# Optimization experiments

Hardware: AMD Instinct MI355X
Metric: run time of the kernel (lower is better)

The kernel has to match this reference:

```python
import jax, jax.numpy as jnp
import numpy as np
from jax import lax


def _conv(x, w, b):
    # x: [B, Cin, H, W], w: [Cout, Cin, 3, 3] -> [B, Cout, H, W] (SAME padding)
    y = lax.conv_general_dilated(x, w, (1, 1), 'SAME',
                                 dimension_numbers=('NCHW', 'OIHW', 'NCHW'))
    return y + b[None, :, None, None]


def _cell_step(h, c, x, w, b):
    gates = _conv(jnp.concatenate([x, h], axis=1), w, b)  # [B, 4, H, W]
    i, f, o, g = jnp.split(gates, 4, axis=1)
    c = jax.nn.sigmoid(f) * c + jax.nn.sigmoid(i) * jnp.tanh(g)
    h = jax.nn.sigmoid(o) * jnp.tanh(c)
    return h, c


def setup_inputs() -> dict:
    key = jax.random.key(0)
    k1, k2, k3 = jax.random.split(key, 3)
    T, B, C, H, W = 20, 1, 1, 1024, 1024
    data = jax.random.normal(k1, (T, B, C, H, W), dtype=jnp.float32)
    enc_w = jax.random.normal(k2, (4, 2, 3, 3), dtype=jnp.float32) * 0.3
    enc_b = jnp.zeros((4,), dtype=jnp.float32)
    dec_w = jax.random.normal(k3, (4, 2, 3, 3), dtype=jnp.float32) * 0.3
    dec_b = jnp.zeros((4,), dtype=jnp.float32)
    return {"data": data, "enc_w": enc_w, "enc_b": enc_b,
            "dec_w": dec_w, "dec_b": dec_b,
            "epoch": 0, "T_en": 20, "T_de": 20}


def reference(data, enc_w, enc_b, dec_w, dec_b, epoch, T_en, T_de):
    B, C, H, W = data.shape[1:]
    h0 = jnp.zeros((B, C, H, W), dtype=data.dtype)
    c0 = jnp.zeros((B, C, H, W), dtype=data.dtype)

    def enc_step(carry, x):
        h, c = _cell_step(carry[0], carry[1], x, enc_w, enc_b)
        return (h, c), None

    (h_enc, _), _ = lax.scan(enc_step, (h0, c0), data[epoch:T_en])

    # decoder_input = encoder_h[0][:, None, :, :] -> with B=C=1 this is h_enc itself
    dec_in = h_enc[0][:, None, :, :]  # [1, 1, H, W]

    def dec_step(carry, _):
        h, c = _cell_step(carry[0], carry[1], dec_in, dec_w, dec_b)
        return (h, c), None

    (h_dec, _), _ = lax.scan(dec_step, (h0, c0), None, length=T_de)
    return h_dec[0, 0]  # [H, W]
```

## Files before the change

kernel.cpp:

```cpp
#include <hip/hip_runtime.h>

#define W 1024
#define H 1024
#define PADX 16
#define PADY 8
#define XS 1056
#define YS 1040
#define FR ((size_t)XS * (size_t)YS)
#define NPIX (H * W)
#define TROWS 32
#define TCOLS 64
#define LRN 48
#define LCV 96
#define LCW 128
#define LBUF (LRN * LCW)
#define NSLOT 460
#define NB 512
#define LOG2E 1.4426950408889634f
#define TWOL  2.8853900817779268f

typedef float v2f __attribute__((ext_vector_type(2)));

__device__ __forceinline__ float frcp_(float v) { return __builtin_amdgcn_rcpf(v); }
__device__ __forceinline__ float exp2_(float v) { return __builtin_amdgcn_exp2f(v); }

__device__ __forceinline__ int swz(int row, int col) {
    return row * LCW + ((((col >> 3) ^ row) & 15) << 3) + (col & 7);
}

__global__ __launch_bounds__(256) void init_ws(const float* __restrict__ ew,
                                               const float* __restrict__ eb,
                                               const float* __restrict__ dw,
                                               const float* __restrict__ db,
                                               float* __restrict__ ws) {
    const size_t n4 = 6 * (FR / 4);
    size_t i = (size_t)blockIdx.x * blockDim.x + threadIdx.x;
    const size_t stride = (size_t)gridDim.x * blockDim.x;
    float4* w4 = (float4*)ws;
    const float4 z = make_float4(0.f, 0.f, 0.f, 0.f);
    for (; i < n4; i += stride) w4[i] = z;
    if (blockIdx.x == 0) {
        float* wsc = ws + 6 * FR;
        const int t = threadIdx.x;
        if (t < 72)                   wsc[t] = ew[t] * ((t / 18 == 3) ? TWOL : LOG2E);
        else if (t < 76)              wsc[t] = eb[t - 72] * ((t - 72 == 3) ? TWOL : LOG2E);
        else if (t >= 80 && t < 152)  wsc[t] = dw[t - 80] * (((t - 80) / 18 == 3) ? TWOL : LOG2E);
        else if (t >= 152 && t < 156) wsc[t] = db[t - 152] * ((t - 152 == 3) ? TWOL : LOG2E);
    }
}

__device__ __forceinline__ void acc_row(float4 A, float4 Bq, float lm, float rp,
                                        const float* __restrict__ wg, int wofs, int dy,
                                        v2f acc[4][4]) {
    const v2f E0 = {A.x, A.y},  E1 = {A.z, A.w};
    const v2f E2 = {Bq.x, Bq.y}, E3 = {Bq.z, Bq.w};
    const v2f O0 = {lm, A.x},   O1 = {A.y, A.z};
    const v2f O2 = {A.w, Bq.x}, O3 = {Bq.y, Bq.z}, O4 = {Bq.w, rp};
#pragma unroll
    for (int co = 0; co < 4; ++co) {
        const float w0 = wg[co * 18 + wofs + dy * 3 + 0];
        const float w1 = wg[co * 18 + wofs + dy * 3 + 1];
        const float w2 = wg[co * 18 + wofs + dy * 3 + 2];
        const v2f W0 = {w0, w0}, W1 = {w1, w1}, W2 = {w2, w2};
        acc[co][0] += W0 * O0 + W1 * E0 + W2 * O1;
        acc[co][1] += W0 * O1 + W1 * E1 + W2 * O2;
        acc[co][2] += W0 * O2 + W1 * E2 + W2 * O3;
        acc[co][3] += W0 * O3 + W1 * E3 + W2 * O4;
    }
}

__device__ __forceinline__ void conv3x8_pk(const float* __restrict__ p, int stride,
                                           const float* __restrict__ wg, int wofs,
                                           v2f acc[4][4]) {
#pragma unroll
    for (int dy = 0; dy < 3; ++dy) {
        acc_row(*(const float4*)p, *(const float4*)(p + 4), p[-1], p[8], wg, wofs, dy, acc);
        p += stride;
    }
}

__device__ __forceinline__ void conv3x8_edge(const float* __restrict__ base, int gr, int gc0,
                                             const float* __restrict__ wg, int wofs,
                                             v2f acc[4][4]) {
    const bool colA = (unsigned)gc0 < (unsigned)W;
    const bool lmok = (unsigned)(gc0 - 1) < (unsigned)W;
    const bool rpok = (unsigned)(gc0 + 8) < (unsigned)W;
#pragma unroll
    for (int dy = 0; dy < 3; ++dy) {
        const int ry = gr - 1 + dy;
        const bool rok = (unsigned)ry < (unsigned)H;
        const float* row = base + (long)ry * W;
        float4 A = make_float4(0.f, 0.f, 0.f, 0.f);
        float4 Bq = make_float4(0.f, 0.f, 0.f, 0.f);
        float lm = 0.f, rp = 0.f;
        if (rok) {
            if (colA) { A = *(const float4*)(row + gc0); Bq = *(const float4*)(row + gc0 + 4); }
            if (lmok) lm = row[gc0 - 1];
            if (rpok) rp = row[gc0 + 8];
        }
        acc_row(A, Bq, lm, rp, wg, wofs, dy, acc);
    }
}

template<int NSTEPS, bool XC>
__global__ __launch_bounds__(NB)
__attribute__((amdgpu_waves_per_eu(4, 4)))
void fusedN(const float* __restrict__ xbase, size_t xstep,
            const float* __restrict__ hin, const float* __restrict__ cin,
            float* __restrict__ hout, float* __restrict__ cout_,
            const float* __restrict__ wg, const float* __restrict__ bg,
            float* __restrict__ dout, int zero_init)
{
    __shared__ float hT[2 * LBUF];
    const int tid = threadIdx.x;
    const int c0 = (blockIdx.x & 15) * TCOLS;
    const int r0 = (blockIdx.x >> 4) * TROWS;

    const bool has = tid < NSLOT;
    const int q   = tid / 10;
    const int jj  = tid - q * 10;
    const int lr  = 1 + q;
    const int lc  = 8 + 8 * jj;
    const int gr  = r0 - 8 + lr;
    const int gc0 = c0 - 8 + 8 * jj;
    const size_t gofs = (size_t)(gr + PADY) * XS + (gc0 + PADX);
    const bool inimg = ((unsigned)gr < (unsigned)H) && ((unsigned)gc0 < (unsigned)W);
    const bool safe = (r0 >= 8) && (r0 + 40 <= H) && (c0 >= 16) && (c0 + 80 <= W);

    for (int idx = tid; idx < LRN * (LCV / 4); idx += NB) {
        const int r = idx / (LCV / 4);
        const int k = idx - r * (LCV / 4);
        float4 v = make_float4(0.f, 0.f, 0.f, 0.f);
        if (!zero_init)
            v = *(const float4*)(hin + (size_t)(r0 + r) * XS + (c0 + 4 * k));
        const int p = swz(r, 4 * k);
        *(float4*)(&hT[p])        = v;
        *(float4*)(&hT[LBUF + p]) = make_float4(0.f, 0.f, 0.f, 0.f);
    }

    float cc[8];
    if (has && !zero_init) {
        const float4 a = *(const float4*)(cin + gofs);
        const float4 b = *(const float4*)(cin + gofs + 4);
        cc[0] = a.x; cc[1] = a.y; cc[2] = a.z; cc[3] = a.w;
        cc[4] = b.x; cc[5] = b.y; cc[6] = b.z; cc[7] = b.w;
    } else {
#pragma unroll
        for (int e = 0; e < 8; ++e) cc[e] = 0.f;
    }

    const int o0 = swz(lr - 1, lc), o0l = swz(lr - 1, lc - 1), o0r = swz(lr - 1, lc + 8);
    const int o1 = swz(lr,     lc), o1l = swz(lr,     lc - 1), o1r = swz(lr,     lc + 8);
    const int o2 = swz(lr + 1, lc), o2l = swz(lr + 1, lc - 1), o2r = swz(lr + 1, lc + 8);

    v2f xacc[4][4];
    if constexpr (XC) {
        if (has) {
#pragma unroll
            for (int co = 0; co < 4; ++co) {
                const v2f bb = {bg[co], bg[co]};
#pragma unroll
                for (int j = 0; j < 4; ++j) xacc[co][j] = bb;
            }
            conv3x8_pk(xbase + gofs - XS, XS, wg, 0, xacc);
        }
    }
    __syncthreads();

    float hh[8];
#pragma unroll
    for (int e = 0; e < 8; ++e) hh[e] = 0.f;

#pragma unroll
    for (int i = 1; i <= NSTEPS; ++i) {
        const float* hR = hT + ((i + 1) & 1) * LBUF;
        float* hW       = hT + (i & 1) * LBUF;
        const bool act = has && (lr >= i) && (lr < LRN - i);
        if (act) {
            const float4 A0 = *(const float4*)(hR + o0);
            const float4 B0 = *(const float4*)(hR + o0 + 4);
            const float4 A1 = *(const float4*)(hR + o1);
            const float4 B1 = *(const float4*)(hR + o1 + 4);
            const float4 A2 = *(const float4*)(hR + o2);
            const float4 B2 = *(const float4*)(hR + o2 + 4);
            const float L0 = hR[o0l], P0 = hR[o0r];
            const float L1 = hR[o1l], P1 = hR[o1r];
            const float L2 = hR[o2l], P2 = hR[o2r];

            v2f acc[4][4];
            if constexpr (XC) {
#pragma unroll
                for (int co = 0; co < 4; ++co)
#pragma unroll
                    for (int j = 0; j < 4; ++j) acc[co][j] = xacc[co][j];
            } else {
#pragma unroll
                for (int co = 0; co < 4; ++co) {
                    const v2f bb = {bg[co], bg[co]};
#pragma unroll
                    for (int j = 0; j < 4; ++j) acc[co][j] = bb;
                }
                const float* xp = xbase + (size_t)(i - 1) * xstep;
                if (safe)
                    conv3x8_pk(xp + (size_t)(gr - 1) * W + gc0, W, wg, 0, acc);
                else
                    conv3x8_edge(xp, gr, gc0, wg, 0, acc);
            }
            acc_row(A0, B0, L0, P0, wg, 9, 0, acc);
            acc_row(A1, B1, L1, P1, wg, 9, 1, acc);
            acc_row(A2, B2, L2, P2, wg, 9, 2, acc);

#pragma unroll
            for (int jp = 0; jp < 4; ++jp) {
#pragma unroll
                for (int s = 0; s < 2; ++s) {
                    const int e = 2 * jp + s;
                    const float Ei = exp2_(-acc[0][jp][s]);
                    const float Ef = exp2_(-acc[1][jp][s]);
                    const float Eo = exp2_(-acc[2][jp][s]);
                    const float Eg = exp2_(acc[3][jp][s]);
                    const float Pp = (1.f + Eg) * (1.f + Ei);
                    const float Qq = 1.f + Ef;
                    const float cn = (cc[e] * Pp + (Eg - 1.f) * Qq) * frcp_(Pp * Qq);
                    cc[e] = cn;
                    const float Ec = exp2_(TWOL * cn);
                    const float hv = (Ec - 1.f) * frcp_((1.f + Eo) * (1.f + Ec));
                    hh[e] = inimg ? hv : 0.f;
                }
            }
            *(float4*)(hW + o1)     = make_float4(hh[0], hh[1], hh[2], hh[3]);
            *(float4*)(hW + o1 + 4) = make_float4(hh[4], hh[5], hh[6], hh[7]);
        }
        __syncthreads();
    }

    if (has && lr >= 8 && lr < 8 + TROWS && jj >= 1 && jj <= 8) {
        if (dout) {
            const size_t o = (size_t)gr * W + gc0;
            *(float4*)(dout + o)     = make_float4(hh[0], hh[1], hh[2], hh[3]);
            *(float4*)(dout + o + 4) = make_float4(hh[4], hh[5], hh[6], hh[7]);
        } else {
            *(float4*)(hout + gofs)      = make_float4(hh[0], hh[1], hh[2], hh[3]);
            *(float4*)(hout + gofs + 4)  = make_float4(hh[4], hh[5], hh[6], hh[7]);
            *(float4*)(cout_ + gofs)     = make_float4(cc[0], cc[1], cc[2], cc[3]);
            *(float4*)(cout_ + gofs + 4) = make_float4(cc[4], cc[5], cc[6], cc[7]);
        }
    }
}

extern "C" void kernel_launch(void* const* d_in, const int* in_sizes, int n_in,
                              void* d_out, int out_size, void* d_ws, size_t ws_size,
                              hipStream_t stream) {
    const float* data  = (const float*)d_in[0];
    const float* enc_w = (const float*)d_in[1];
    const float* enc_b = (const float*)d_in[2];
    const float* dec_w = (const float*)d_in[3];
    const float* dec_b = (const float*)d_in[4];

    float* ws  = (float*)d_ws;
    float* hE1 = ws + 0 * FR;
    float* cE1 = ws + 1 * FR;
    float* hE0 = ws + 2 * FR;
    float* cE0 = ws + 3 * FR;
    float* hX  = ws + 4 * FR;
    float* cX  = ws + 5 * FR;
    float* wsc = ws + 6 * FR;
    const float* encW = wsc;
    const float* encB = wsc + 72;
    const float* decW = wsc + 80;
    const float* decB = wsc + 152;
    float* dout = (float*)d_out;

    init_ws<<<2048, 256, 0, stream>>>(enc_w, enc_b, dec_w, dec_b, ws);

    dim3 blk(NB), grd(512);
    fusedN<8, false><<<grd, blk, 0, stream>>>(data,                     (size_t)NPIX,
                                              nullptr, nullptr, hE1, cE1, encW, encB, nullptr, 1);
    fusedN<8, false><<<grd, blk, 0, stream>>>(data + (size_t)8 * NPIX,  (size_t)NPIX,
                                              hE1, cE1, hE0, cE0, encW, encB, nullptr, 0);
    fusedN<4, false><<<grd, blk, 0, stream>>>(data + (size_t)16 * NPIX, (size_t)NPIX,
                                              hE0, cE0, hE1, cE1, encW, encB, nullptr, 0);
    fusedN<8, true><<<grd, blk, 0, stream>>>(hE1, 0, nullptr, nullptr,
                                             hE0, cE0, decW, decB, nullptr, 1);
    fusedN<8, true><<<grd, blk, 0, stream>>>(hE1, 0, hE0, cE0,
                                             hX,  cX,  decW, decB, nullptr, 0);
    fusedN<4, true><<<grd, blk, 0, stream>>>(hE1, 0, hX,  cX,
                                             nullptr, nullptr, decW, decB, dout, 0);
}
```

Measured before the change: 393.6 us.

## Switch to 4-step temporal tiles with smaller 16x64 spatial tiles

Restructures the temporally fused ConvLSTM kernels from 8-step chunks over 32x64 tiles to 4-step chunks over 16x64 tiles with a 4-pixel halo. Each thread now handles 4 pixels instead of 8, and blocks are smaller (448 threads, 1024 blocks) with higher waves-per-EU. The LDS layout becomes padded rows without swizzling, and the pipeline grows from 6 to 10 kernel launches. The aim is less redundant halo recomputation per step and better occupancy, at the cost of more launches and more global h/c round trips.

```diff
diff --git a/kernel.cpp b/kernel.cpp
--- a/kernel.cpp
+++ b/kernel.cpp
@@ -2,20 +2,21 @@
 
 #define W 1024
 #define H 1024
-#define PADX 16
-#define PADY 8
-#define XS 1056
-#define YS 1040
+#define PAD 4
+#define XS 1032
+#define YS 1032
 #define FR ((size_t)XS * (size_t)YS)
 #define NPIX (H * W)
-#define TROWS 32
-#define TCOLS 64
-#define LRN 48
-#define LCV 96
-#define LCW 128
-#define LBUF (LRN * LCW)
-#define NSLOT 460
-#define NB 512
+#define TRR 16
+#define TCC 64
+#define NBX 16
+#define NBY 64
+#define RROWS 24
+#define RCOLS 72
+#define LST 80
+#define LBUF (RROWS * LST)
+#define NSLOT 396
+#define NT 448
 #define LOG2E 1.4426950408889634f
 #define TWOL  2.8853900817779268f
 
@@ -23,24 +24,20 @@
 
 __device__ __forceinline__ float frcp_(float v) { return __builtin_amdgcn_rcpf(v); }
 __device__ __forceinline__ float exp2_(float v) { return __builtin_amdgcn_exp2f(v); }
-
-__device__ __forceinline__ int swz(int row, int col) {
-    return row * LCW + ((((col >> 3) ^ row) & 15) << 3) + (col & 7);
-}
 
 __global__ __launch_bounds__(256) void init_ws(const float* __restrict__ ew,
                                                const float* __restrict__ eb,
                                                const float* __restrict__ dw,
                                                const float* __restrict__ db,
                                                float* __restrict__ ws) {
-    const size_t n4 = 6 * (FR / 4);
+    const size_t n4 = (XS + 6 * FR) / 4;
     size_t i = (size_t)blockIdx.x * blockDim.x + threadIdx.x;
     const size_t stride = (size_t)gridDim.x * blockDim.x;
     float4* w4 = (float4*)ws;
     const float4 z = make_float4(0.f, 0.f, 0.f, 0.f);
     for (; i < n4; i += stride) w4[i] = z;
     if (blockIdx.x == 0) {
-        float* wsc = ws + 6 * FR;
+        float* wsc = ws + XS + 6 * FR;
         const int t = threadIdx.x;
         if (t < 72)                   wsc[t] = ew[t] * ((t / 18 == 3) ? TWOL : LOG2E);
         else if (t < 76)              wsc[t] = eb[t - 72] * ((t - 72 == 3) ? TWOL : LOG2E);
@@ -49,63 +46,38 @@
     }
 }
 
-__device__ __forceinline__ void acc_row(float4 A, float4 Bq, float lm, float rp,
-                                        const float* __restrict__ wg, int wofs, int dy,
-                                        v2f acc[4][4]) {
-    const v2f E0 = {A.x, A.y},  E1 = {A.z, A.w};
-    const v2f E2 = {Bq.x, Bq.y}, E3 = {Bq.z, Bq.w};
-    const v2f O0 = {lm, A.x},   O1 = {A.y, A.z};
-    const v2f O2 = {A.w, Bq.x}, O3 = {Bq.y, Bq.z}, O4 = {Bq.w, rp};
+__device__ __forceinline__ void acc_row4(float lm, float4 m, float rp,
+                                         const float* __restrict__ wg, int wofs,
+                                         v2f acc[4][2]) {
+    const v2f E0 = {m.x, m.y}, E1 = {m.z, m.w};
+    const v2f O0 = {lm, m.x}, O1 = {m.y, m.z}, O2 = {m.w, rp};
 #pragma unroll
     for (int co = 0; co < 4; ++co) {
-        const float w0 = wg[co * 18 + wofs + dy * 3 + 0];
-        const float w1 = wg[co * 18 + wofs + dy * 3 + 1];
-        const float w2 = wg[co * 18 + wofs + dy * 3 + 2];
+        const float w0 = wg[co * 18 + wofs + 0];
+        const float w1 = wg[co * 18 + wofs + 1];
+        const float w2 = wg[co * 18 + wofs + 2];
         const v2f W0 = {w0, w0}, W1 = {w1, w1}, W2 = {w2, w2};
         acc[co][0] += W0 * O0 + W1 * E0 + W2 * O1;
         acc[co][1] += W0 * O1 + W1 * E1 + W2 * O2;
-        acc[co][2] += W0 * O2 + W1 * E2 + W2 * O3;
-        acc[co][3] += W0 * O3 + W1 * E3 + W2 * O4;
-    }
-}
-
-__device__ __forceinline__ void conv3x8_pk(const float* __restrict__ p, int stride,
-                                           const float* __restrict__ wg, int wofs,
-                                           v2f acc[4][4]) {
-#pragma unroll
-    for (int dy = 0; dy < 3; ++dy) {
-        acc_row(*(const float4*)p, *(const float4*)(p + 4), p[-1], p[8], wg, wofs, dy, acc);
-        p += stride;
-    }
-}
-
-__device__ __forceinline__ void conv3x8_edge(const float* __restrict__ base, int gr, int gc0,
-                                             const float* __restrict__ wg, int wofs,
-                                             v2f acc[4][4]) {
-    const bool colA = (unsigned)gc0 < (unsigned)W;
-    const bool lmok = (unsigned)(gc0 - 1) < (unsigned)W;
-    const bool rpok = (unsigned)(gc0 + 8) < (unsigned)W;
-#pragma unroll
-    for (int dy = 0; dy < 3; ++dy) {
-        const int ry = gr - 1 + dy;
-        const bool rok = (unsigned)ry < (unsigned)H;
-        const float* row = base + (long)ry * W;
-        float4 A = make_float4(0.f, 0.f, 0.f, 0.f);
-        float4 Bq = make_float4(0.f, 0.f, 0.f, 0.f);
-        float lm = 0.f, rp = 0.f;
-        if (rok) {
-            if (colA) { A = *(const float4*)(row + gc0); Bq = *(const float4*)(row + gc0 + 4); }
-            if (lmok) lm = row[gc0 - 1];
-            if (rpok) rp = row[gc0 + 8];
-        }
-        acc_row(A, Bq, lm, rp, wg, wofs, dy, acc);
-    }
-}
-
-template<int NSTEPS, bool XC>
-__global__ __launch_bounds__(NB)
-__attribute__((amdgpu_waves_per_eu(4, 4)))
-void fusedN(const float* __restrict__ xbase, size_t xstep,
+    }
+}
+
+struct XR { float lm; float4 m; float rp; };
+__device__ __forceinline__ XR ldx4(const float* __restrict__ fr, int ry, int gc0) {
+    XR r; r.m = make_float4(0.f, 0.f, 0.f, 0.f); r.lm = 0.f; r.rp = 0.f;
+    if ((unsigned)ry < (unsigned)H) {
+        const float* p = fr + (size_t)ry * W + gc0;
+        if ((unsigned)gc0 < (unsigned)W)       r.m  = *(const float4*)p;
+        if ((unsigned)(gc0 - 1) < (unsigned)W) r.lm = p[-1];
+        if ((unsigned)(gc0 + 4) < (unsigned)W) r.rp = p[4];
+    }
+    return r;
+}
+
+template<bool XC>
+__global__ __launch_bounds__(NT)
+__attribute__((amdgpu_waves_per_eu(6, 7)))
+void fused4(const float* __restrict__ xbase, size_t xstep,
             const float* __restrict__ hin, const float* __restrict__ cin,
             float* __restrict__ hout, float* __restrict__ cout_,
             const float* __restrict__ wg, const float* __restrict__ bg,
@@ -113,105 +85,111 @@
 {
     __shared__ float hT[2 * LBUF];
     const int tid = threadIdx.x;
-    const int c0 = (blockIdx.x & 15) * TCOLS;
-    const int r0 = (blockIdx.x >> 4) * TROWS;
+    const int bx = blockIdx.x & (NBX - 1);
+    const int by = blockIdx.x >> 4;
+    const int c0 = bx * TCC, r0 = by * TRR;
 
     const bool has = tid < NSLOT;
-    const int q   = tid / 10;
-    const int jj  = tid - q * 10;
-    const int lr  = 1 + q;
-    const int lc  = 8 + 8 * jj;
-    const int gr  = r0 - 8 + lr;
-    const int gc0 = c0 - 8 + 8 * jj;
-    const size_t gofs = (size_t)(gr + PADY) * XS + (gc0 + PADX);
+    const int q    = tid / 18;
+    const int g    = tid - q * 18;
+    const int lrow = 1 + q;
+    const int lcol = 4 * g;
+    const int gr   = r0 - PAD + lrow;
+    const int gc0  = c0 - PAD + lcol;
+    const size_t gofs = (size_t)(gr + PAD) * XS + (gc0 + PAD);
     const bool inimg = ((unsigned)gr < (unsigned)H) && ((unsigned)gc0 < (unsigned)W);
-    const bool safe = (r0 >= 8) && (r0 + 40 <= H) && (c0 >= 16) && (c0 + 80 <= W);
-
-    for (int idx = tid; idx < LRN * (LCV / 4); idx += NB) {
-        const int r = idx / (LCV / 4);
-        const int k = idx - r * (LCV / 4);
+    const bool safe = (r0 >= 4) && (r0 + 20 <= H) && (c0 >= 5) && (c0 + 69 <= W);
+
+    for (int idx = tid; idx < 2 * RROWS * (LST / 4); idx += NT) {
+        const int b   = idx / (RROWS * (LST / 4));
+        const int k   = idx - b * (RROWS * (LST / 4));
+        const int row = k / (LST / 4);
+        const int ch  = k - row * (LST / 4);
         float4 v = make_float4(0.f, 0.f, 0.f, 0.f);
-        if (!zero_init)
-            v = *(const float4*)(hin + (size_t)(r0 + r) * XS + (c0 + 4 * k));
-        const int p = swz(r, 4 * k);
-        *(float4*)(&hT[p])        = v;
-        *(float4*)(&hT[LBUF + p]) = make_float4(0.f, 0.f, 0.f, 0.f);
-    }
-
-    float cc[8];
+        if (b == 0 && !zero_init && ch >= 1 && ch <= 18)
+            v = *(const float4*)(hin + (size_t)(r0 + row) * XS + (c0 + 4 * (ch - 1)));
+        *(float4*)(&hT[b * LBUF + row * LST + 4 * ch]) = v;
+    }
+
+    float cc[4], hh[4];
     if (has && !zero_init) {
         const float4 a = *(const float4*)(cin + gofs);
-        const float4 b = *(const float4*)(cin + gofs + 4);
         cc[0] = a.x; cc[1] = a.y; cc[2] = a.z; cc[3] = a.w;
-        cc[4] = b.x; cc[5] = b.y; cc[6] = b.z; cc[7] = b.w;
     } else {
 #pragma unroll
-        for (int e = 0; e < 8; ++e) cc[e] = 0.f;
-    }
-
-    const int o0 = swz(lr - 1, lc), o0l = swz(lr - 1, lc - 1), o0r = swz(lr - 1, lc + 8);
-    const int o1 = swz(lr,     lc), o1l = swz(lr,     lc - 1), o1r = swz(lr,     lc + 8);
-    const int o2 = swz(lr + 1, lc), o2l = swz(lr + 1, lc - 1), o2r = swz(lr + 1, lc + 8);
-
-    v2f xacc[4][4];
+        for (int e = 0; e < 4; ++e) cc[e] = 0.f;
+    }
+#pragma unroll
+    for (int e = 0; e < 4; ++e) hh[e] = 0.f;
+
+    v2f xacc[4][2];
     if constexpr (XC) {
         if (has) {
 #pragma unroll
             for (int co = 0; co < 4; ++co) {
                 const v2f bb = {bg[co], bg[co]};
-#pragma unroll
-                for (int j = 0; j < 4; ++j) xacc[co][j] = bb;
+                xacc[co][0] = bb; xacc[co][1] = bb;
             }
-            conv3x8_pk(xbase + gofs - XS, XS, wg, 0, xacc);
+            const float* p = xbase + gofs - XS;
+            acc_row4(p[-1], *(const float4*)p, p[4], wg, 0, xacc);
+            p += XS;
+            acc_row4(p[-1], *(const float4*)p, p[4], wg, 3, xacc);
+            p += XS;
+            acc_row4(p[-1], *(const float4*)p, p[4], wg, 6, xacc);
         }
     }
     __syncthreads();
 
-    float hh[8];
-#pragma unroll
-    for (int e = 0; e < 8; ++e) hh[e] = 0.f;
-
-#pragma unroll
-    for (int i = 1; i <= NSTEPS; ++i) {
+#pragma unroll
+    for (int i = 1; i <= 4; ++i) {
         const float* hR = hT + ((i + 1) & 1) * LBUF;
         float* hW       = hT + (i & 1) * LBUF;
-        const bool act = has && (lr >= i) && (lr < LRN - i);
+        const bool act = has && (lrow >= i) && (lrow < RROWS - i);
         if (act) {
+            const int o1 = lrow * LST + 4 + lcol;
+            const int o0 = o1 - LST, o2 = o1 + LST;
             const float4 A0 = *(const float4*)(hR + o0);
-            const float4 B0 = *(const float4*)(hR + o0 + 4);
             const float4 A1 = *(const float4*)(hR + o1);
-            const float4 B1 = *(const float4*)(hR + o1 + 4);
             const float4 A2 = *(const float4*)(hR + o2);
-            const float4 B2 = *(const float4*)(hR + o2 + 4);
-            const float L0 = hR[o0l], P0 = hR[o0r];
-            const float L1 = hR[o1l], P1 = hR[o1r];
-            const float L2 = hR[o2l], P2 = hR[o2r];
-
-            v2f acc[4][4];
+            const float L0 = hR[o0 - 1], P0 = hR[o0 + 4];
+            const float L1 = hR[o1 - 1], P1 = hR[o1 + 4];
+            const float L2 = hR[o2 - 1], P2 = hR[o2 + 4];
+
+            v2f acc[4][2];
             if constexpr (XC) {
 #pragma unroll
-                for (int co = 0; co < 4; ++co)
-#pragma unroll
-                    for (int j = 0; j < 4; ++j) acc[co][j] = xacc[co][j];
+                for (int co = 0; co < 4; ++co) {
+                    acc[co][0] = xacc[co][0]; acc[co][1] = xacc[co][1];
+                }
             } else {
 #pragma unroll
                 for (int co = 0; co < 4; ++co) {
                     const v2f bb = {bg[co], bg[co]};
-#pragma unroll
-                    for (int j = 0; j < 4; ++j) acc[co][j] = bb;
-                }
-                const float* xp = xbase + (size_t)(i - 1) * xstep;
-                if (safe)
-                    conv3x8_pk(xp + (size_t)(gr - 1) * W + gc0, W, wg, 0, acc);
-                else
-                    conv3x8_edge(xp, gr, gc0, wg, 0, acc);
+                    acc[co][0] = bb; acc[co][1] = bb;
+                }
+                const float* xf = xbase + (size_t)(i - 1) * xstep;
+                if (safe) {
+                    const float* p = xf + (size_t)(gr - 1) * W + gc0;
+                    acc_row4(p[-1], *(const float4*)p, p[4], wg, 0, acc);
+                    p += W;
+                    acc_row4(p[-1], *(const float4*)p, p[4], wg, 3, acc);
+                    p += W;
+                    acc_row4(p[-1], *(const float4*)p, p[4], wg, 6, acc);
+                } else {
+                    const XR x0 = ldx4(xf, gr - 1, gc0);
+                    acc_row4(x0.lm, x0.m, x0.rp, wg, 0, acc);
+                    const XR x1 = ldx4(xf, gr, gc0);
+                    acc_row4(x1.lm, x1.m, x1.rp, wg, 3, acc);
+                    const XR x2 = ldx4(xf, gr + 1, gc0);
+                    acc_row4(x2.lm, x2.m, x2.rp, wg, 6, acc);
+                }
             }
-            acc_row(A0, B0, L0, P0, wg, 9, 0, acc);
-            acc_row(A1, B1, L1, P1, wg, 9, 1, acc);
-            acc_row(A2, B2, L2, P2, wg, 9, 2, acc);
-
-#pragma unroll
-            for (int jp = 0; jp < 4; ++jp) {
+            acc_row4(L0, A0, P0, wg, 9, acc);
+            acc_row4(L1, A1, P1, wg, 12, acc);
+            acc_row4(L2, A2, P2, wg, 15, acc);
+
+#pragma unroll
+            for (int jp = 0; jp < 2; ++jp) {
 #pragma unroll
                 for (int s = 0; s < 2; ++s) {
                     const int e = 2 * jp + s;
@@ -228,22 +206,18 @@
                     hh[e] = inimg ? hv : 0.f;
                 }
             }
-            *(float4*)(hW + o1)     = make_float4(hh[0], hh[1], hh[2], hh[3]);
-            *(float4*)(hW + o1 + 4) = make_float4(hh[4], hh[5], hh[6], hh[7]);
+            *(float4*)(hW + o1) = make_float4(hh[0], hh[1], hh[2], hh[3]);
         }
         __syncthreads();
     }
 
-    if (has && lr >= 8 && lr < 8 + TROWS && jj >= 1 && jj <= 8) {
+    if (has && lrow >= PAD && lrow < PAD + TRR && g >= 1 && g <= 16) {
         if (dout) {
-            const size_t o = (size_t)gr * W + gc0;
-            *(float4*)(dout + o)     = make_float4(hh[0], hh[1], hh[2], hh[3]);
-            *(float4*)(dout + o + 4) = make_float4(hh[4], hh[5], hh[6], hh[7]);
+            *(float4*)(dout + (size_t)gr * W + gc0) =
+                make_float4(hh[0], hh[1], hh[2], hh[3]);
         } else {
-            *(float4*)(hout + gofs)      = make_float4(hh[0], hh[1], hh[2], hh[3]);
-            *(float4*)(hout + gofs + 4)  = make_float4(hh[4], hh[5], hh[6], hh[7]);
-            *(float4*)(cout_ + gofs)     = make_float4(cc[0], cc[1], cc[2], cc[3]);
-            *(float4*)(cout_ + gofs + 4) = make_float4(cc[4], cc[5], cc[6], cc[7]);
+            *(float4*)(hout + gofs)  = make_float4(hh[0], hh[1], hh[2], hh[3]);
+            *(float4*)(cout_ + gofs) = make_float4(cc[0], cc[1], cc[2], cc[3]);
         }
     }
 }
@@ -258,13 +232,14 @@
     const float* dec_b = (const float*)d_in[4];
 
     float* ws  = (float*)d_ws;
-    float* hE1 = ws + 0 * FR;
-    float* cE1 = ws + 1 * FR;
-    float* hE0 = ws + 2 * FR;
-    float* cE0 = ws + 3 * FR;
-    float* hX  = ws + 4 * FR;
-    float* cX  = ws + 5 * FR;
-    float* wsc = ws + 6 * FR;
+    float* sb  = ws + XS;
+    float* hE1 = sb + 0 * FR;
+    float* cE1 = sb + 1 * FR;
+    float* hE0 = sb + 2 * FR;
+    float* cE0 = sb + 3 * FR;
+    float* hX  = sb + 4 * FR;
+    float* cX  = sb + 5 * FR;
+    float* wsc = sb + 6 * FR;
     const float* encW = wsc;
     const float* encB = wsc + 72;
     const float* decW = wsc + 80;
@@ -273,17 +248,26 @@
 
     init_ws<<<2048, 256, 0, stream>>>(enc_w, enc_b, dec_w, dec_b, ws);
 
-    dim3 blk(NB), grd(512);
-    fusedN<8, false><<<grd, blk, 0, stream>>>(data,                     (size_t)NPIX,
-                                              nullptr, nullptr, hE1, cE1, encW, encB, nullptr, 1);
-    fusedN<8, false><<<grd, blk, 0, stream>>>(data + (size_t)8 * NPIX,  (size_t)NPIX,
-                                              hE1, cE1, hE0, cE0, encW, encB, nullptr, 0);
-    fusedN<4, false><<<grd, blk, 0, stream>>>(data + (size_t)16 * NPIX, (size_t)NPIX,
-                                              hE0, cE0, hE1, cE1, encW, encB, nullptr, 0);
-    fusedN<8, true><<<grd, blk, 0, stream>>>(hE1, 0, nullptr, nullptr,
-                                             hE0, cE0, decW, decB, nullptr, 1);
-    fusedN<8, true><<<grd, blk, 0, stream>>>(hE1, 0, hE0, cE0,
-                                             hX,  cX,  decW, decB, nullptr, 0);
-    fusedN<4, true><<<grd, blk, 0, stream>>>(hE1, 0, hX,  cX,
-                                             nullptr, nullptr, decW, decB, dout, 0);
-}
+    dim3 blk(NT), grd(NBX * NBY);
+    const size_t xf4 = (size_t)4 * NPIX;
+    fused4<false><<<grd, blk, 0, stream>>>(data,           (size_t)NPIX,
+                                           nullptr, nullptr, hE1, cE1, encW, encB, nullptr, 1);
+    fused4<false><<<grd, blk, 0, stream>>>(data + 1 * xf4, (size_t)NPIX,
+                                           hE1, cE1, hE0, cE0, encW, encB, nullptr, 0);
+    fused4<false><<<grd, blk, 0, stream>>>(data + 2 * xf4, (size_t)NPIX,
+                                           hE0, cE0, hE1, cE1, encW, encB, nullptr, 0);
+    fused4<false><<<grd, blk, 0, stream>>>(data + 3 * xf4, (size_t)NPIX,
+                                           hE1, cE1, hE0, cE0, encW, encB, nullptr, 0);
+    fused4<false><<<grd, blk, 0, stream>>>(data + 4 * xf4, (size_t)NPIX,
+                                           hE0, cE0, hE1, cE1, encW, encB, nullptr, 0);
+    fused4<true><<<grd, blk, 0, stream>>>(hE1, 0, nullptr, nullptr,
+                                          hX, cX, decW, decB, nullptr, 1);
+    fused4<true><<<grd, blk, 0, stream>>>(hE1, 0, hX, cX,
+                                          hE0, cE0, decW, decB, nullptr, 0);
+    fused4<true><<<grd, blk, 0, stream>>>(hE1, 0, hE0, cE0,
+                                          hX, cX, decW, decB, nullptr, 0);
+    fused4<true><<<grd, blk, 0, stream>>>(hE1, 0, hX, cX,
+                                          hE0, cE0, decW, decB, nullptr, 0);
+    fused4<true><<<grd, blk, 0, stream>>>(hE1, 0, hE0, cE0,
+                                          nullptr, nullptr, decW, decB, dout, 0);
+}
```

New measurement: 465.7 us. 1.18x slower.
